# Performance work log

Measured on AMD Instinct MI355X. Metric: run time of the kernel, lower is better.

The kernel has to match this reference:

```python
import jax, jax.numpy as jnp
import numpy as np

B, Q, V, H, U = 4, 256, 2048, 512, 128

def setup_inputs() -> dict:
    key = jax.random.key(0)
    ks = jax.random.split(key, 5)
    return {
        "queries": jax.random.normal(ks[0], (B, Q, H), dtype=jnp.float32),
        "values": jax.random.normal(ks[1], (B, V, H), dtype=jnp.float32),
        "w1": jax.random.normal(ks[2], (H, U), dtype=jnp.float32) / np.sqrt(H),
        "w2": jax.random.normal(ks[3], (H, U), dtype=jnp.float32) / np.sqrt(H),
        "v": jax.random.normal(ks[4], (U,), dtype=jnp.float32) / np.sqrt(U),
    }

def reference(queries, values, w1, w2, v):
    # Project queries and values first (cheap GEMMs), then broadcast-add.
    pq = jnp.einsum("bqh,hu->bqu", queries, w1)          # [B,Q,U]
    pv = jnp.einsum("bvh,hu->bvu", values, w2)           # [B,V,U]
    # added_qv: [B,Q,V,U] -- the large intermediate the original materializes
    scores = jnp.einsum("bqvu,u->bqv", jnp.tanh(pq[:, :, None, :] + pv[:, None, :, :]), v)
    attn = jax.nn.softmax(scores, axis=-1)               # softmax over V (last axis, as tf.nn.softmax)
    return jnp.einsum("bqv,bvh->bqh", attn, values)      # [B,Q,H]
```

## Files before the change

kernel.cpp:

```cpp
#include <hip/hip_runtime.h>

#define BB 4
#define QQ 256
#define VV 2048
#define HH 512
#define UU 128

#define C2E   2.8853900817779268f
#define LOG2E 1.4426950408889634f

__device__ __forceinline__ void fma4(float4& a, float s, const float4& w) {
    a.x = fmaf(s, w.x, a.x);
    a.y = fmaf(s, w.y, a.y);
    a.z = fmaf(s, w.z, a.z);
    a.w = fmaf(s, w.w, a.w);
}
__device__ __forceinline__ float2 rcp2(float2 x) {
    return make_float2(__builtin_amdgcn_rcpf(x.x), __builtin_amdgcn_rcpf(x.y));
}
__device__ __forceinline__ float2 mul2(float2 a, float2 b) { return make_float2(a.x*b.x, a.y*b.y); }
__device__ __forceinline__ float2 muls(float2 a, float s)  { return make_float2(a.x*s, a.y*s); }
__device__ __forceinline__ float2 fma2(float2 a, float2 b, float2 c) {
    return make_float2(fmaf(a.x, b.x, c.x), fmaf(a.y, b.y, c.y));
}
__device__ __forceinline__ float2 fmas(float2 a, float s, float2 c) {
    return make_float2(fmaf(a.x, s, c.x), fmaf(a.y, s, c.y));
}

__global__ __launch_bounds__(256) void proj_kernel(const float* __restrict__ queries,
                                                   const float* __restrict__ values,
                                                   const float* __restrict__ w1,
                                                   const float* __restrict__ w2,
                                                   float* __restrict__ pqI,
                                                   float* __restrict__ pvI,
                                                   float* __restrict__ denom) {
    __shared__ float smem[32 * 36 + 32 * 128];
    float (*As)[36] = (float(*)[36])smem;
    float* Ws = smem + 32 * 36;
    float (*Ls)[36] = (float(*)[36])smem;

    const int bid = blockIdx.x;
    const int tid = threadIdx.x;
    if (bid == 0) *(float4*)&denom[tid * 4] = make_float4(0.f, 0.f, 0.f, 0.f);

    const bool isv = (bid < 256);
    const float* A; const float* W; int b, r0, ROWS; float* Ob;
    if (isv) {
        b = bid >> 6; r0 = (bid & 63) * 32;
        A = values + ((size_t)(b * VV + r0)) * HH;  W = w2;
        Ob = pvI + (size_t)b * UU * VV;  ROWS = VV;
    } else {
        const int q = bid - 256;
        b = q >> 3; r0 = (q & 7) * 32;
        A = queries + ((size_t)(b * QQ + r0)) * HH; W = w1;
        Ob = pqI + (size_t)b * UU * QQ;  ROWS = QQ;
    }

    const int tx = tid & 31;
    const int ty = tid >> 5;
    float4 acc[4];
#pragma unroll
    for (int j = 0; j < 4; j++) acc[j] = make_float4(0.f, 0.f, 0.f, 0.f);

    for (int k0 = 0; k0 < HH; k0 += 32) {
        {
            const int r = tid >> 3, kk4 = (tid & 7) * 4;
            const float4 a = *(const float4*)&A[(size_t)r * HH + k0 + kk4];
            As[kk4 + 0][r] = a.x; As[kk4 + 1][r] = a.y;
            As[kk4 + 2][r] = a.z; As[kk4 + 3][r] = a.w;
        }
#pragma unroll
        for (int t = 0; t < 4; t++) {
            const int f = tid + t * 256;
            const int kk = f >> 5, u4 = (f & 31) * 4;
            *(float4*)&Ws[kk * 128 + u4] = *(const float4*)&W[(size_t)(k0 + kk) * UU + u4];
        }
        __syncthreads();
#pragma unroll
        for (int kk = 0; kk < 32; kk++) {
            const float4 a = *(const float4*)&As[kk][ty * 4];
            const float4 w = *(const float4*)&Ws[kk * 128 + tx * 4];
            fma4(acc[0], a.x, w);
            fma4(acc[1], a.y, w);
            fma4(acc[2], a.z, w);
            fma4(acc[3], a.w, w);
        }
        __syncthreads();
    }
#pragma unroll
    for (int j = 0; j < 4; j++) {
        const float aa[4] = {acc[j].x, acc[j].y, acc[j].z, acc[j].w};
#pragma unroll
        for (int i = 0; i < 4; i++)
            Ls[tx * 4 + i][ty * 4 + j] = __builtin_amdgcn_exp2f(aa[i] * C2E);
    }
    __syncthreads();
#pragma unroll
    for (int t = 0; t < 4; t++) {
        const int idx = tid + t * 256;
        const int g = idx >> 5, r = idx & 31;
        float4 o;
        o.x = Ls[4 * g + 0][r]; o.y = Ls[4 * g + 1][r];
        o.z = Ls[4 * g + 2][r]; o.w = Ls[4 * g + 3][r];
        *(float4*)&Ob[((size_t)g * ROWS + r0 + r) * 4] = o;
    }
}

__global__ __launch_bounds__(256, 4) void fused_kernel(const float* __restrict__ pqI,
                                                       const float* __restrict__ pvI,
                                                       const float* __restrict__ vvec,
                                                       const float* __restrict__ values,
                                                       float* __restrict__ slab,
                                                       float* __restrict__ denom) {
    __shared__ float att[128][16];
    __shared__ float wred[2][16];
    const int tid = threadIdx.x;
    const int bid = blockIdx.x;
    const int vs = bid & 15, qb = (bid >> 4) & 15, b = bid >> 8;
    const int qbase = qb * 16, vbase = vs * 128;

    const int vloc = tid & 127, uh = tid >> 7;
    const int v = vbase + vloc;

    float vsum = 0.0f;
#pragma unroll
    for (int u4 = 0; u4 < UU; u4 += 4) {
        const float4 t = *(const float4*)&vvec[u4];
        vsum += t.x + t.y + t.z + t.w;
    }

    const float* pv4 = pvI + (size_t)b * UU * VV + (size_t)v * 4;
    const float* pq4 = pqI + (size_t)b * UU * QQ + (size_t)qbase * 4;

    float2 acc[8];
#pragma unroll
    for (int p = 0; p < 8; p++) acc[p] = make_float2(0.f, 0.f);

    const int G0 = uh * 16;
    float4 ev = *(const float4*)&pv4[(size_t)G0 * VV * 4];

    for (int g = 0; g < 16; g++) {
        const int G = G0 + g;
        const float* eqp = &pq4[(size_t)G * QQ * 4];
        float4 evn;
        if (g < 15) evn = *(const float4*)&pv4[(size_t)(G + 1) * VV * 4];
        const float4 wq = *(const float4*)&vvec[G * 4];
        const float w0 = 2.f * wq.x, w1 = 2.f * wq.y;
        const float w2 = 2.f * wq.z, w3 = 2.f * wq.w;
#pragma unroll
        for (int p = 0; p < 8; p++) {
            const float4 e0 = *(const float4*)&eqp[(2 * p) * 4];
            const float4 e1 = *(const float4*)&eqp[(2 * p + 1) * 4];
            const float2 a1 = make_float2(fmaf(e0.x, ev.x, 1.f), fmaf(e1.x, ev.x, 1.f));
            const float2 b1 = make_float2(fmaf(e0.y, ev.y, 1.f), fmaf(e1.y, ev.y, 1.f));
            const float2 c1 = make_float2(fmaf(e0.z, ev.z, 1.f), fmaf(e1.z, ev.z, 1.f));
            const float2 d1 = make_float2(fmaf(e0.w, ev.w, 1.f), fmaf(e1.w, ev.w, 1.f));
            const float2 pab = mul2(a1, b1), pcd = mul2(c1, d1);
            const float2 nab = fmas(a1, w1, muls(b1, w0));
            const float2 ncd = fmas(c1, w3, muls(d1, w2));
            const float2 num = fma2(nab, pcd, mul2(ncd, pab));
            const float2 den = mul2(pab, pcd);
            acc[p] = fma2(num, rcp2(den), acc[p]);
        }
        ev = evn;
    }

    if (uh == 1) {
#pragma unroll
        for (int p = 0; p < 8; p++)
            *(float2*)&att[vloc][2 * p] = acc[p];
    }
    __syncthreads();
    if (uh == 0) {
#pragma unroll
        for (int p = 0; p < 8; p++) {
            const float2 hi = *(const float2*)&att[vloc][2 * p];
            float2 e;
            e.x = __builtin_amdgcn_exp2f((vsum - (acc[p].x + hi.x)) * LOG2E);
            e.y = __builtin_amdgcn_exp2f((vsum - (acc[p].y + hi.y)) * LOG2E);
            *(float2*)&att[vloc][2 * p] = e;
            acc[p] = e;
        }
#pragma unroll
        for (int off = 1; off < 64; off <<= 1) {
#pragma unroll
            for (int p = 0; p < 8; p++) {
                acc[p].x += __shfl_xor(acc[p].x, off, 64);
                acc[p].y += __shfl_xor(acc[p].y, off, 64);
            }
        }
        if ((tid & 63) == 0) {
            const int w = tid >> 6;
#pragma unroll
            for (int p = 0; p < 8; p++) {
                wred[w][2 * p + 0] = acc[p].x;
                wred[w][2 * p + 1] = acc[p].y;
            }
        }
    }
    __syncthreads();
    if (tid < 16)
        atomicAdd(&denom[b * QQ + qbase + tid], wred[0][tid] + wred[1][tid]);

    const int hg = tid & 127, qh = tid >> 7;
    const int h0 = hg * 4;
    const float* vp = values + ((size_t)(b * VV + vbase)) * HH + h0;

    float4 oacc[8];
#pragma unroll
    for (int j = 0; j < 8; j++) oacc[j] = make_float4(0.f, 0.f, 0.f, 0.f);

#pragma unroll 2
    for (int vv = 0; vv < 128; vv++) {
        const float4 w = *(const float4*)&vp[(size_t)vv * HH];
        const float4 a0 = *(const float4*)&att[vv][qh * 8 + 0];
        const float4 a1 = *(const float4*)&att[vv][qh * 8 + 4];
        fma4(oacc[0], a0.x, w); fma4(oacc[1], a0.y, w);
        fma4(oacc[2], a0.z, w); fma4(oacc[3], a0.w, w);
        fma4(oacc[4], a1.x, w); fma4(oacc[5], a1.y, w);
        fma4(oacc[6], a1.z, w); fma4(oacc[7], a1.w, w);
    }

    float* sp = slab + (size_t)vs * (BB * QQ * HH);
#pragma unroll
    for (int j = 0; j < 8; j++) {
        const int q = qh * 8 + j;
        *(float4*)&sp[((size_t)(b * QQ + qbase + q)) * HH + h0] = oacc[j];
    }
}

__global__ __launch_bounds__(256) void reduce_kernel(const float* __restrict__ slab,
                                                     const float* __restrict__ denom,
                                                     float* __restrict__ out) {
    const int i = blockIdx.x * 256 + threadIdx.x;
    const float r = __builtin_amdgcn_rcpf(denom[i >> 7]);
    const float4* s4 = (const float4*)slab;
    float4 s = s4[i];
#pragma unroll
    for (int k = 1; k < 16; k++) {
        const float4 p = s4[(size_t)k * (BB * QQ * HH / 4) + i];
        s.x += p.x; s.y += p.y; s.z += p.z; s.w += p.w;
    }
    s.x *= r; s.y *= r; s.z *= r; s.w *= r;
    ((float4*)out)[i] = s;
}

extern "C" void kernel_launch(void* const* d_in, const int* in_sizes, int n_in,
                              void* d_out, int out_size, void* d_ws, size_t ws_size,
                              hipStream_t stream) {
    const float* queries = (const float*)d_in[0];
    const float* values  = (const float*)d_in[1];
    const float* w1      = (const float*)d_in[2];
    const float* w2      = (const float*)d_in[3];
    const float* vvec    = (const float*)d_in[4];
    float* out = (float*)d_out;

    float* ws    = (float*)d_ws;
    float* pqI   = ws;
    float* pvI   = pqI + BB * UU * QQ;
    float* denom = pvI + (size_t)BB * UU * VV;
    float* slab  = denom + BB * QQ;

    proj_kernel<<<256 + 32, 256, 0, stream>>>(queries, values, w1, w2, pqI, pvI, denom);
    fused_kernel<<<BB * (QQ / 16) * (VV / 128), 256, 0, stream>>>(pqI, pvI, vvec, values, slab, denom);
    reduce_kernel<<<(BB * QQ * HH) / 4 / 256, 256, 0, stream>>>(slab, denom, out);
}
```

Measured before the change: 173.9 us.

## Fuse split-V reduction into fused kernel via last-block atomic counter

Removes the separate reduce kernel launch. Each (batch, q-block) tile now keeps an atomic counter, and the last of its 16 V-split blocks to finish sums the slab partials, applies the softmax normalization and writes the output. This saves one kernel launch and lets the reduction overlap with other blocks still computing. In exchange it adds fences and atomics, and the final reduction runs serially inside only 64 blocks, which may create tail latency.

```diff
diff --git a/kernel.cpp b/kernel.cpp
--- a/kernel.cpp
+++ b/kernel.cpp
@@ -33,7 +33,8 @@
                                                    const float* __restrict__ w2,
                                                    float* __restrict__ pqI,
                                                    float* __restrict__ pvI,
-                                                   float* __restrict__ denom) {
+                                                   float* __restrict__ denom,
+                                                   int* __restrict__ cnt) {
     __shared__ float smem[32 * 36 + 32 * 128];
     float (*As)[36] = (float(*)[36])smem;
     float* Ws = smem + 32 * 36;
@@ -41,7 +42,10 @@
 
     const int bid = blockIdx.x;
     const int tid = threadIdx.x;
-    if (bid == 0) *(float4*)&denom[tid * 4] = make_float4(0.f, 0.f, 0.f, 0.f);
+    if (bid == 0) {
+        *(float4*)&denom[tid * 4] = make_float4(0.f, 0.f, 0.f, 0.f);
+        if (tid < 64) cnt[tid] = 0;
+    }
 
     const bool isv = (bid < 256);
     const float* A; const float* W; int b, r0, ROWS; float* Ob;
@@ -111,9 +115,12 @@
                                                        const float* __restrict__ vvec,
                                                        const float* __restrict__ values,
                                                        float* __restrict__ slab,
-                                                       float* __restrict__ denom) {
+                                                       float* __restrict__ denom,
+                                                       int* __restrict__ cnt,
+                                                       float* __restrict__ out) {
     __shared__ float att[128][16];
     __shared__ float wred[2][16];
+    __shared__ int lastFlag;
     const int tid = threadIdx.x;
     const int bid = blockIdx.x;
     const int vs = bid & 15, qb = (bid >> 4) & 15, b = bid >> 8;
@@ -227,22 +234,33 @@
         const int q = qh * 8 + j;
         *(float4*)&sp[((size_t)(b * QQ + qbase + q)) * HH + h0] = oacc[j];
     }
-}
-
-__global__ __launch_bounds__(256) void reduce_kernel(const float* __restrict__ slab,
-                                                     const float* __restrict__ denom,
-                                                     float* __restrict__ out) {
-    const int i = blockIdx.x * 256 + threadIdx.x;
-    const float r = __builtin_amdgcn_rcpf(denom[i >> 7]);
+
+    __syncthreads();
+    if (tid == 0) {
+        __threadfence();
+        lastFlag = (atomicAdd(&cnt[b * 16 + qb], 1) == 15);
+    }
+    __syncthreads();
+    if (!lastFlag) return;
+    __threadfence();
+
+    const float* dn = denom + b * QQ + qbase;
     const float4* s4 = (const float4*)slab;
-    float4 s = s4[i];
-#pragma unroll
-    for (int k = 1; k < 16; k++) {
-        const float4 p = s4[(size_t)k * (BB * QQ * HH / 4) + i];
-        s.x += p.x; s.y += p.y; s.z += p.z; s.w += p.w;
-    }
-    s.x *= r; s.y *= r; s.z *= r; s.w *= r;
-    ((float4*)out)[i] = s;
+#pragma unroll
+    for (int j = 0; j < 8; j++) {
+        const int i = tid + j * 256;
+        const int q = i >> 7, h4 = i & 127;
+        const size_t off = ((size_t)(b * QQ + qbase + q)) * (HH / 4) + h4;
+        float4 s = make_float4(0.f, 0.f, 0.f, 0.f);
+#pragma unroll
+        for (int k = 0; k < 16; k++) {
+            const float4 p = s4[(size_t)k * (BB * QQ * HH / 4) + off];
+            s.x += p.x; s.y += p.y; s.z += p.z; s.w += p.w;
+        }
+        const float r = __builtin_amdgcn_rcpf(dn[q]);
+        s.x *= r; s.y *= r; s.z *= r; s.w *= r;
+        ((float4*)out)[off] = s;
+    }
 }
 
 extern "C" void kernel_launch(void* const* d_in, const int* in_sizes, int n_in,
@@ -259,9 +277,10 @@
     float* pqI   = ws;
     float* pvI   = pqI + BB * UU * QQ;
     float* denom = pvI + (size_t)BB * UU * VV;
-    float* slab  = denom + BB * QQ;
-
-    proj_kernel<<<256 + 32, 256, 0, stream>>>(queries, values, w1, w2, pqI, pvI, denom);
-    fused_kernel<<<BB * (QQ / 16) * (VV / 128), 256, 0, stream>>>(pqI, pvI, vvec, values, slab, denom);
-    reduce_kernel<<<(BB * QQ * HH) / 4 / 256, 256, 0, stream>>>(slab, denom, out);
-}
+    int*   cnt   = (int*)(denom + BB * QQ);
+    float* slab  = denom + BB * QQ + 64;
+
+    proj_kernel<<<256 + 32, 256, 0, stream>>>(queries, values, w1, w2, pqI, pvI, denom, cnt);
+    fused_kernel<<<BB * (QQ / 16) * (VV / 128), 256, 0, stream>>>(pqI, pvI, vvec, values,
+                                                                  slab, denom, cnt, out);
+}
```

Result: slower. 265.2 us (+52.5%).

## Remap PV accumulation to 2 columns x 16 queries; halve projection tile rows

Applied to the files above, without the earlier changes.

In the fused kernel's attention-times-values stage, each thread now accumulates 2 hidden columns for all 16 queries instead of 4 columns for 8 queries. Each value row is then read from global memory once per block rather than by two thread halves, while the attention weights come from shared-memory broadcasts. The projection kernel moves to 16-row tiles with 128 threads, doubling the block count for better occupancy across CUs. The costs are more LDS reads per FMA, narrower float2 global accesses, and more redundant weight-tile loads in the projection.

```diff
diff --git a/kernel.cpp b/kernel.cpp
--- a/kernel.cpp
+++ b/kernel.cpp
@@ -15,6 +15,10 @@
     a.z = fmaf(s, w.z, a.z);
     a.w = fmaf(s, w.w, a.w);
 }
+__device__ __forceinline__ void fma2s(float2& a, float s, const float2& w) {
+    a.x = fmaf(s, w.x, a.x);
+    a.y = fmaf(s, w.y, a.y);
+}
 __device__ __forceinline__ float2 rcp2(float2 x) {
     return make_float2(__builtin_amdgcn_rcpf(x.x), __builtin_amdgcn_rcpf(x.y));
 }
@@ -27,31 +31,34 @@
     return make_float2(fmaf(a.x, s, c.x), fmaf(a.y, s, c.y));
 }
 
-__global__ __launch_bounds__(256) void proj_kernel(const float* __restrict__ queries,
+__global__ __launch_bounds__(128) void proj_kernel(const float* __restrict__ queries,
                                                    const float* __restrict__ values,
                                                    const float* __restrict__ w1,
                                                    const float* __restrict__ w2,
                                                    float* __restrict__ pqI,
                                                    float* __restrict__ pvI,
                                                    float* __restrict__ denom) {
-    __shared__ float smem[32 * 36 + 32 * 128];
-    float (*As)[36] = (float(*)[36])smem;
-    float* Ws = smem + 32 * 36;
-    float (*Ls)[36] = (float(*)[36])smem;
+    __shared__ float smem[32 * 20 + 32 * 128];
+    float (*As)[20] = (float(*)[20])smem;
+    float* Ws = smem + 32 * 20;
+    float (*Ls)[20] = (float(*)[20])smem;
 
     const int bid = blockIdx.x;
     const int tid = threadIdx.x;
-    if (bid == 0) *(float4*)&denom[tid * 4] = make_float4(0.f, 0.f, 0.f, 0.f);
-
-    const bool isv = (bid < 256);
+    if (bid == 0) {
+        *(float4*)&denom[tid * 8]     = make_float4(0.f, 0.f, 0.f, 0.f);
+        *(float4*)&denom[tid * 8 + 4] = make_float4(0.f, 0.f, 0.f, 0.f);
+    }
+
+    const bool isv = (bid < 512);
     const float* A; const float* W; int b, r0, ROWS; float* Ob;
     if (isv) {
-        b = bid >> 6; r0 = (bid & 63) * 32;
+        b = bid >> 7; r0 = (bid & 127) * 16;
         A = values + ((size_t)(b * VV + r0)) * HH;  W = w2;
         Ob = pvI + (size_t)b * UU * VV;  ROWS = VV;
     } else {
-        const int q = bid - 256;
-        b = q >> 3; r0 = (q & 7) * 32;
+        const int q = bid - 512;
+        b = q >> 4; r0 = (q & 15) * 16;
         A = queries + ((size_t)(b * QQ + r0)) * HH; W = w1;
         Ob = pqI + (size_t)b * UU * QQ;  ROWS = QQ;
     }
@@ -70,8 +77,8 @@
             As[kk4 + 2][r] = a.z; As[kk4 + 3][r] = a.w;
         }
 #pragma unroll
-        for (int t = 0; t < 4; t++) {
-            const int f = tid + t * 256;
+        for (int t = 0; t < 8; t++) {
+            const int f = tid + t * 128;
             const int kk = f >> 5, u4 = (f & 31) * 4;
             *(float4*)&Ws[kk * 128 + u4] = *(const float4*)&W[(size_t)(k0 + kk) * UU + u4];
         }
@@ -97,8 +104,8 @@
     __syncthreads();
 #pragma unroll
     for (int t = 0; t < 4; t++) {
-        const int idx = tid + t * 256;
-        const int g = idx >> 5, r = idx & 31;
+        const int idx = tid + t * 128;
+        const int g = idx >> 4, r = idx & 15;
         float4 o;
         o.x = Ls[4 * g + 0][r]; o.y = Ls[4 * g + 1][r];
         o.z = Ls[4 * g + 2][r]; o.w = Ls[4 * g + 3][r];
@@ -202,30 +209,34 @@
     if (tid < 16)
         atomicAdd(&denom[b * QQ + qbase + tid], wred[0][tid] + wred[1][tid]);
 
-    const int hg = tid & 127, qh = tid >> 7;
-    const int h0 = hg * 4;
+    const int h0 = tid * 2;
     const float* vp = values + ((size_t)(b * VV + vbase)) * HH + h0;
 
-    float4 oacc[8];
-#pragma unroll
-    for (int j = 0; j < 8; j++) oacc[j] = make_float4(0.f, 0.f, 0.f, 0.f);
+    float2 oacc[16];
+#pragma unroll
+    for (int j = 0; j < 16; j++) oacc[j] = make_float2(0.f, 0.f);
 
 #pragma unroll 2
     for (int vv = 0; vv < 128; vv++) {
-        const float4 w = *(const float4*)&vp[(size_t)vv * HH];
-        const float4 a0 = *(const float4*)&att[vv][qh * 8 + 0];
-        const float4 a1 = *(const float4*)&att[vv][qh * 8 + 4];
-        fma4(oacc[0], a0.x, w); fma4(oacc[1], a0.y, w);
-        fma4(oacc[2], a0.z, w); fma4(oacc[3], a0.w, w);
-        fma4(oacc[4], a1.x, w); fma4(oacc[5], a1.y, w);
-        fma4(oacc[6], a1.z, w); fma4(oacc[7], a1.w, w);
+        const float2 w = *(const float2*)&vp[(size_t)vv * HH];
+        const float4 a0 = *(const float4*)&att[vv][0];
+        const float4 a1 = *(const float4*)&att[vv][4];
+        const float4 a2 = *(const float4*)&att[vv][8];
+        const float4 a3 = *(const float4*)&att[vv][12];
+        fma2s(oacc[0],  a0.x, w); fma2s(oacc[1],  a0.y, w);
+        fma2s(oacc[2],  a0.z, w); fma2s(oacc[3],  a0.w, w);
+        fma2s(oacc[4],  a1.x, w); fma2s(oacc[5],  a1.y, w);
+        fma2s(oacc[6],  a1.z, w); fma2s(oacc[7],  a1.w, w);
+        fma2s(oacc[8],  a2.x, w); fma2s(oacc[9],  a2.y, w);
+        fma2s(oacc[10], a2.z, w); fma2s(oacc[11], a2.w, w);
+        fma2s(oacc[12], a3.x, w); fma2s(oacc[13], a3.y, w);
+        fma2s(oacc[14], a3.z, w); fma2s(oacc[15], a3.w, w);
     }
 
     float* sp = slab + (size_t)vs * (BB * QQ * HH);
 #pragma unroll
-    for (int j = 0; j < 8; j++) {
-        const int q = qh * 8 + j;
-        *(float4*)&sp[((size_t)(b * QQ + qbase + q)) * HH + h0] = oacc[j];
+    for (int j = 0; j < 16; j++) {
+        *(float2*)&sp[((size_t)(b * QQ + qbase + j)) * HH + h0] = oacc[j];
     }
 }
 
@@ -261,7 +272,8 @@
     float* denom = pvI + (size_t)BB * UU * VV;
     float* slab  = denom + BB * QQ;
 
-    proj_kernel<<<256 + 32, 256, 0, stream>>>(queries, values, w1, w2, pqI, pvI, denom);
-    fused_kernel<<<BB * (QQ / 16) * (VV / 128), 256, 0, stream>>>(pqI, pvI, vvec, values, slab, denom);
+    proj_kernel<<<512 + 64, 128, 0, stream>>>(queries, values, w1, w2, pqI, pvI, denom);
+    fused_kernel<<<BB * (QQ / 16) * (VV / 128), 256, 0, stream>>>(pqI, pvI, vvec, values,
+                                                                  slab, denom);
     reduce_kernel<<<(BB * QQ * HH) / 4 / 256, 256, 0, stream>>>(slab, denom, out);
 }
```

Result: slower. 177.4 us (+2.0%).
